# Performance work log

Measured on AMD Instinct MI355X. Metric: run time of the kernel, lower is better.

## Reference

```python
import jax, jax.numpy as jnp
import numpy as np

N_NODES = 100000


def _degrees(idx, n):
    d = jax.ops.segment_sum(jnp.ones(idx.shape[0], jnp.float32), idx, num_segments=n)
    return jnp.maximum(d, 1.0)  # DGL clamps zero degrees to 1


def graph_conv(src, dst, x, W, b, n):
    # DGL GraphConv with norm='both': out = D_in^{-1/2} A D_out^{-1/2} x W + b
    norm_src = _degrees(src, n) ** -0.5  # out-degree of source nodes
    norm_dst = _degrees(dst, n) ** -0.5  # in-degree of destination nodes
    xs = x * norm_src[:, None]
    msgs = xs[src]                                    # [E, d] gather
    agg = jax.ops.segment_sum(msgs, dst, num_segments=n)  # [N, d] scatter-add
    agg = agg * norm_dst[:, None]
    return agg @ W + b


def setup_inputs() -> dict:
    key = jax.random.key(0)
    k = jax.random.split(key, 7)
    E = 1600000
    in_f, h_f, out_f = 128, 128, 64
    return {
        "in_feat": jax.random.normal(k[0], (N_NODES, in_f), jnp.float32),
        "src": jax.random.randint(k[1], (E,), 0, N_NODES, jnp.int32),
        "dst": jax.random.randint(k[2], (E,), 0, N_NODES, jnp.int32),
        "W1": jax.random.normal(k[3], (in_f, h_f), jnp.float32) * (1.0 / np.sqrt(in_f)),
        "b1": jnp.zeros((h_f,), jnp.float32),
        "W2": jax.random.normal(k[4], (h_f, out_f), jnp.float32) * (1.0 / np.sqrt(h_f)),
        "b2": jnp.zeros((out_f,), jnp.float32),
    }


def reference(in_feat, src, dst, W1, b1, W2, b2):
    h = graph_conv(src, dst, in_feat, W1, b1, N_NODES)
    h = jax.nn.relu(h)
    h = graph_conv(src, dst, h, W2, b2, N_NODES)
    return h
```

## Files before the change

### kernel.cpp

```cpp
#include <hip/hip_runtime.h>

#define SLOT_CAP 64
#define NB_MAX 1024

__device__ __forceinline__ unsigned int bf16_rne(float f) {
    unsigned int u = __float_as_uint(f);
    return (u + 0x7FFFu + ((u >> 16) & 1u)) >> 16;
}
__device__ __forceinline__ unsigned int pack2(float a, float b) {
    return bf16_rne(a) | (bf16_rne(b) << 16);
}
__device__ __forceinline__ float bflo(unsigned int u) { return __uint_as_float(u << 16); }
__device__ __forceinline__ float bfhi(unsigned int u) { return __uint_as_float(u & 0xFFFF0000u); }

__global__ __launch_bounds__(256) void ka_kernel(
    const float* __restrict__ A, const float* __restrict__ W,
    unsigned short* __restrict__ C, int M,
    const int* __restrict__ src, const int* __restrict__ dst,
    int* __restrict__ bucket_cnt,
    int E, int GB, int NB)
{
    __shared__ __align__(16) int smem[32 * 68 + 32 * 128];
    const int tid = threadIdx.x;
    const int bid = blockIdx.x;

    if (bid >= GB) {
        const int eb = bid - GB;
        for (int b = tid; b < 2 * NB; b += 256) smem[b] = 0;
        __syncthreads();
        const int base = eb * 8192;
#pragma unroll
        for (int it = 0; it < 8; it++) {
            const int i4 = base + (it * 256 + tid) * 4;
            if (i4 + 3 < E) {
                int4 s = *(const int4*)(src + i4);
                int4 d = *(const int4*)(dst + i4);
                atomicAdd(&smem[d.x >> 7], 1); atomicAdd(&smem[d.y >> 7], 1);
                atomicAdd(&smem[d.z >> 7], 1); atomicAdd(&smem[d.w >> 7], 1);
                atomicAdd(&smem[NB + (s.x >> 7)], 1); atomicAdd(&smem[NB + (s.y >> 7)], 1);
                atomicAdd(&smem[NB + (s.z >> 7)], 1); atomicAdd(&smem[NB + (s.w >> 7)], 1);
            } else {
                for (int i = i4; i < E && i < i4 + 4; i++) {
                    atomicAdd(&smem[dst[i] >> 7], 1);
                    atomicAdd(&smem[NB + (src[i] >> 7)], 1);
                }
            }
        }
        __syncthreads();
        for (int b = tid; b < 2 * NB; b += 256) {
            int v = smem[b];
            if (v) atomicAdd(&bucket_cnt[b], v);
        }
        return;
    }

    float (*As2)[68] = (float(*)[68])smem;
    float* Ws = (float*)(smem + 32 * 68);
    const int row0 = bid * 64;
    if (row0 >= M) return;
    const int cx = tid & 31;
    const int ry = tid >> 5;
    const int kk = tid & 31;
    const int ri = tid >> 5;

    float acc[8][4];
#pragma unroll
    for (int r = 0; r < 8; r++)
#pragma unroll
        for (int c = 0; c < 4; c++) acc[r][c] = 0.0f;

    for (int k0 = 0; k0 < 128; k0 += 32) {
        __syncthreads();
#pragma unroll
        for (int jj = 0; jj < 8; jj++) {
            int r = ri + 8 * jj;
            int row = row0 + r;
            float v = 0.0f;
            if (row < M) v = A[(size_t)row * 128 + k0 + kk];
            As2[kk][r] = v;
        }
#pragma unroll
        for (int jj = 0; jj < 16; jj++) {
            int idx = tid + 256 * jj;
            Ws[idx] = W[k0 * 128 + idx];
        }
        __syncthreads();
#pragma unroll
        for (int k = 0; k < 32; k++) {
            float4 w = *(const float4*)&Ws[k * 128 + cx * 4];
            const float* ap = &As2[k][ry * 8];
            float4 a0 = *(const float4*)ap;
            float4 a1 = *(const float4*)(ap + 4);
            float a[8] = {a0.x, a0.y, a0.z, a0.w, a1.x, a1.y, a1.z, a1.w};
#pragma unroll
            for (int r = 0; r < 8; r++) {
                acc[r][0] = fmaf(a[r], w.x, acc[r][0]);
                acc[r][1] = fmaf(a[r], w.y, acc[r][1]);
                acc[r][2] = fmaf(a[r], w.z, acc[r][2]);
                acc[r][3] = fmaf(a[r], w.w, acc[r][3]);
            }
        }
    }
#pragma unroll
    for (int r = 0; r < 8; r++) {
        int row = row0 + ry * 8 + r;
        if (row < M) {
            uint2 p;
            p.x = pack2(acc[r][0], acc[r][1]);
            p.y = pack2(acc[r][2], acc[r][3]);
            *(uint2*)&C[(size_t)row * 128 + cx * 4] = p;
        }
    }
}

__global__ __launch_bounds__(256) void prefix_kernel(
    const int* __restrict__ bucket_cnt, int* __restrict__ bucket_base,
    int* __restrict__ bucket_cursor, int NB)
{
    __shared__ int tsum[256];
    const int off = blockIdx.x * NB;
    const int t = threadIdx.x;
    int v[4];
    int s = 0;
#pragma unroll
    for (int j = 0; j < 4; j++) {
        int b = t * 4 + j;
        v[j] = (b < NB) ? bucket_cnt[off + b] : 0;
        s += v[j];
    }
    tsum[t] = s;
    __syncthreads();
    for (int o = 1; o < 256; o <<= 1) {
        int x = (t >= o) ? tsum[t - o] : 0;
        __syncthreads();
        tsum[t] += x;
        __syncthreads();
    }
    int running = tsum[t] - s;
#pragma unroll
    for (int j = 0; j < 4; j++) {
        int b = t * 4 + j;
        if (b < NB) { bucket_base[off + b] = running; bucket_cursor[off + b] = running; }
        running += v[j];
    }
}

__global__ __launch_bounds__(256) void kb_kernel(
    const int* __restrict__ src, const int* __restrict__ dst,
    int* __restrict__ cursor,
    unsigned int* __restrict__ edge_shuf,
    unsigned char* __restrict__ src_shuf,
    int E, int NB)
{
    __shared__ int cntL[2 * NB_MAX];
    __shared__ int ofsL[2 * NB_MAX];
    const int tid = threadIdx.x;
    const int base = blockIdx.x * 8192;
    for (int b = tid; b < 2 * NB; b += 256) cntL[b] = 0;
    __syncthreads();
#pragma unroll
    for (int it = 0; it < 8; it++) {
        const int i4 = base + (it * 256 + tid) * 4;
        if (i4 + 3 < E) {
            int4 s = *(const int4*)(src + i4);
            int4 d = *(const int4*)(dst + i4);
            atomicAdd(&cntL[d.x >> 7], 1); atomicAdd(&cntL[d.y >> 7], 1);
            atomicAdd(&cntL[d.z >> 7], 1); atomicAdd(&cntL[d.w >> 7], 1);
            atomicAdd(&cntL[NB + (s.x >> 7)], 1); atomicAdd(&cntL[NB + (s.y >> 7)], 1);
            atomicAdd(&cntL[NB + (s.z >> 7)], 1); atomicAdd(&cntL[NB + (s.w >> 7)], 1);
        } else {
            for (int i = i4; i < E && i < i4 + 4; i++) {
                atomicAdd(&cntL[dst[i] >> 7], 1);
                atomicAdd(&cntL[NB + (src[i] >> 7)], 1);
            }
        }
    }
    __syncthreads();
    for (int b = tid; b < 2 * NB; b += 256) {
        int c = cntL[b];
        ofsL[b] = c ? atomicAdd(&cursor[b], c) : 0;
    }
    __syncthreads();
#pragma unroll
    for (int it = 0; it < 8; it++) {
        const int i4 = base + (it * 256 + tid) * 4;
        if (i4 + 3 < E) {
            int4 s = *(const int4*)(src + i4);
            int4 d = *(const int4*)(dst + i4);
            { int p = atomicAdd(&ofsL[d.x >> 7], 1); edge_shuf[p] = (unsigned)s.x | ((unsigned)(d.x & 127) << 17); }
            { int p = atomicAdd(&ofsL[d.y >> 7], 1); edge_shuf[p] = (unsigned)s.y | ((unsigned)(d.y & 127) << 17); }
            { int p = atomicAdd(&ofsL[d.z >> 7], 1); edge_shuf[p] = (unsigned)s.z | ((unsigned)(d.z & 127) << 17); }
            { int p = atomicAdd(&ofsL[d.w >> 7], 1); edge_shuf[p] = (unsigned)s.w | ((unsigned)(d.w & 127) << 17); }
            { int q = atomicAdd(&ofsL[NB + (s.x >> 7)], 1); src_shuf[q] = (unsigned char)(s.x & 127); }
            { int q = atomicAdd(&ofsL[NB + (s.y >> 7)], 1); src_shuf[q] = (unsigned char)(s.y & 127); }
            { int q = atomicAdd(&ofsL[NB + (s.z >> 7)], 1); src_shuf[q] = (unsigned char)(s.z & 127); }
            { int q = atomicAdd(&ofsL[NB + (s.w >> 7)], 1); src_shuf[q] = (unsigned char)(s.w & 127); }
        } else {
            for (int i = i4; i < E && i < i4 + 4; i++) {
                int sv = src[i], dv = dst[i];
                int p = atomicAdd(&ofsL[dv >> 7], 1);
                edge_shuf[p] = (unsigned)sv | ((unsigned)(dv & 127) << 17);
                int q = atomicAdd(&ofsL[NB + (sv >> 7)], 1);
                src_shuf[q] = (unsigned char)(sv & 127);
            }
        }
    }
}

__global__ __launch_bounds__(256) void kc_src_kernel(
    const unsigned char* __restrict__ src_shuf,
    const int* __restrict__ bucket_base, const int* __restrict__ bucket_cnt,
    int* __restrict__ cnt_src, int N)
{
    __shared__ int cntL[128];
    const int tid = threadIdx.x;
    const int b = blockIdx.x;
    if (tid < 128) cntL[tid] = 0;
    __syncthreads();
    const int start = bucket_base[b];
    const int len = bucket_cnt[b];
    for (int i = start + tid; i < start + len; i += 256)
        atomicAdd(&cntL[src_shuf[i]], 1);
    __syncthreads();
    if (tid < 128) {
        int node = b * 128 + tid;
        if (node < N) cnt_src[node] = cntL[tid];
    }
}

__global__ __launch_bounds__(256) void kc_dst_kernel(
    const unsigned int* __restrict__ edge_shuf,
    const int* __restrict__ bucket_base, const int* __restrict__ bucket_cnt,
    const int* __restrict__ cnt_src,
    int* __restrict__ cnt_dst, unsigned int* __restrict__ slots, int N)
{
    __shared__ int cntL[128];
    __shared__ unsigned int slotsL[128 * SLOT_CAP];
    const int tid = threadIdx.x;
    const int b = blockIdx.x;
    if (tid < 128) cntL[tid] = 0;
    __syncthreads();
    const int start = bucket_base[b];
    const int len = bucket_cnt[b];
    for (int i = start + tid; i < start + len; i += 256) {
        unsigned e = edge_shuf[i];
        int d = e >> 17;
        unsigned s = e & 0x1FFFFu;
        unsigned deg = (unsigned)min(cnt_src[s], 255);
        int r = atomicAdd(&cntL[d], 1);
        if (r < SLOT_CAP) slotsL[d * SLOT_CAP + r] = s | (deg << 17);
    }
    __syncthreads();
    if (tid < 128) {
        int node = b * 128 + tid;
        if (node < N) cnt_dst[node] = cntL[tid];
    }
    const int g = tid >> 4, lane = tid & 15;
    for (int nl = g; nl < 128; nl += 16) {
        int node = b * 128 + nl;
        if (node >= N) break;
        int len2 = min(cntL[nl], SLOT_CAP);
        for (int c = 0; c * 16 < len2; c++)
            slots[(size_t)node * SLOT_CAP + c * 16 + lane] = slotsL[nl * SLOT_CAP + c * 16 + lane];
    }
}

#define ACC8(V_, S_) \
    acc[0] = fmaf(bflo((V_).x), (S_), acc[0]); acc[1] = fmaf(bfhi((V_).x), (S_), acc[1]); \
    acc[2] = fmaf(bflo((V_).y), (S_), acc[2]); acc[3] = fmaf(bfhi((V_).y), (S_), acc[3]); \
    acc[4] = fmaf(bflo((V_).z), (S_), acc[4]); acc[5] = fmaf(bfhi((V_).z), (S_), acc[5]); \
    acc[6] = fmaf(bflo((V_).w), (S_), acc[6]); acc[7] = fmaf(bfhi((V_).w), (S_), acc[7]);

#define SUM8(V_) \
    acc[0] += bflo((V_).x); acc[1] += bfhi((V_).x); \
    acc[2] += bflo((V_).y); acc[3] += bfhi((V_).y); \
    acc[4] += bflo((V_).z); acc[5] += bfhi((V_).z); \
    acc[6] += bflo((V_).w); acc[7] += bfhi((V_).w);

__global__ __launch_bounds__(256) void pg2_kernel(
    const int* __restrict__ cnt_src, const int* __restrict__ cnt_dst,
    const unsigned int* __restrict__ slots, const unsigned int* __restrict__ msg,
    const float* __restrict__ W2, const float* __restrict__ b1,
    unsigned short* __restrict__ C, int N)
{
    __shared__ unsigned int Agp[64][66];
    __shared__ float Ws[32 * 64];
    const int tid = threadIdx.x;
    const int m0 = blockIdx.x * 64;
    const int lane = tid & 15;

#pragma unroll
    for (int p = 0; p < 4; p++) {
        const int nl = p * 16 + (tid >> 4);
        const int node = m0 + nl;
        float acc[8];
#pragma unroll
        for (int k = 0; k < 8; k++) acc[k] = 0.0f;
        if (node < N) {
            const unsigned int* sl = slots + (size_t)node * SLOT_CAP;
            const int cd = cnt_dst[node];
            const int len = min(cd, SLOT_CAP);
            int j = 0;
            for (; j + 7 < len; j += 8) {
                uint4 e0 = *(const uint4*)(sl + j);
                uint4 e1 = *(const uint4*)(sl + j + 4);
                uint4 a0 = *(const uint4*)(msg + (size_t)(e0.x & 0x1FFFFu) * 64 + lane * 4);
                uint4 a1 = *(const uint4*)(msg + (size_t)(e0.y & 0x1FFFFu) * 64 + lane * 4);
                uint4 a2 = *(const uint4*)(msg + (size_t)(e0.z & 0x1FFFFu) * 64 + lane * 4);
                uint4 a3 = *(const uint4*)(msg + (size_t)(e0.w & 0x1FFFFu) * 64 + lane * 4);
                uint4 a4 = *(const uint4*)(msg + (size_t)(e1.x & 0x1FFFFu) * 64 + lane * 4);
                uint4 a5 = *(const uint4*)(msg + (size_t)(e1.y & 0x1FFFFu) * 64 + lane * 4);
                uint4 a6 = *(const uint4*)(msg + (size_t)(e1.z & 0x1FFFFu) * 64 + lane * 4);
                uint4 a7 = *(const uint4*)(msg + (size_t)(e1.w & 0x1FFFFu) * 64 + lane * 4);
                float w0 = rsqrtf((float)(e0.x >> 17));
                float w1 = rsqrtf((float)(e0.y >> 17));
                float w2 = rsqrtf((float)(e0.z >> 17));
                float w3 = rsqrtf((float)(e0.w >> 17));
                float w4 = rsqrtf((float)(e1.x >> 17));
                float w5 = rsqrtf((float)(e1.y >> 17));
                float w6 = rsqrtf((float)(e1.z >> 17));
                float w7 = rsqrtf((float)(e1.w >> 17));
                ACC8(a0, w0) ACC8(a1, w1) ACC8(a2, w2) ACC8(a3, w3)
                ACC8(a4, w4) ACC8(a5, w5) ACC8(a6, w6) ACC8(a7, w7)
            }
            for (; j + 3 < len; j += 4) {
                uint4 e0 = *(const uint4*)(sl + j);
                uint4 a0 = *(const uint4*)(msg + (size_t)(e0.x & 0x1FFFFu) * 64 + lane * 4);
                uint4 a1 = *(const uint4*)(msg + (size_t)(e0.y & 0x1FFFFu) * 64 + lane * 4);
                uint4 a2 = *(const uint4*)(msg + (size_t)(e0.z & 0x1FFFFu) * 64 + lane * 4);
                uint4 a3 = *(const uint4*)(msg + (size_t)(e0.w & 0x1FFFFu) * 64 + lane * 4);
                float w0 = rsqrtf((float)(e0.x >> 17));
                float w1 = rsqrtf((float)(e0.y >> 17));
                float w2 = rsqrtf((float)(e0.z >> 17));
                float w3 = rsqrtf((float)(e0.w >> 17));
                ACC8(a0, w0) ACC8(a1, w1) ACC8(a2, w2) ACC8(a3, w3)
            }
            for (; j < len; j++) {
                unsigned e = sl[j];
                uint4 a0 = *(const uint4*)(msg + (size_t)(e & 0x1FFFFu) * 64 + lane * 4);
                float w0 = rsqrtf((float)(e >> 17));
                ACC8(a0, w0)
            }
            float nd = rsqrtf(fmaxf((float)cd, 1.0f));
            float ns = rsqrtf(fmaxf((float)cnt_src[node], 1.0f));
            float4 bA = *(const float4*)(b1 + lane * 8);
            float4 bB = *(const float4*)(b1 + lane * 8 + 4);
            acc[0] = fmaxf(fmaf(nd, acc[0], bA.x), 0.0f) * ns;
            acc[1] = fmaxf(fmaf(nd, acc[1], bA.y), 0.0f) * ns;
            acc[2] = fmaxf(fmaf(nd, acc[2], bA.z), 0.0f) * ns;
            acc[3] = fmaxf(fmaf(nd, acc[3], bA.w), 0.0f) * ns;
            acc[4] = fmaxf(fmaf(nd, acc[4], bB.x), 0.0f) * ns;
            acc[5] = fmaxf(fmaf(nd, acc[5], bB.y), 0.0f) * ns;
            acc[6] = fmaxf(fmaf(nd, acc[6], bB.z), 0.0f) * ns;
            acc[7] = fmaxf(fmaf(nd, acc[7], bB.w), 0.0f) * ns;
        }
        uint4 pk;
        pk.x = pack2(acc[0], acc[1]);
        pk.y = pack2(acc[2], acc[3]);
        pk.z = pack2(acc[4], acc[5]);
        pk.w = pack2(acc[6], acc[7]);
        *(uint4*)&Agp[nl][lane * 4] = pk;
    }
    __syncthreads();

    const int cx = tid & 15;
    const int rg = tid >> 4;
    float acc2[4][4];
#pragma unroll
    for (int r = 0; r < 4; r++)
#pragma unroll
        for (int c = 0; c < 4; c++) acc2[r][c] = 0.0f;

    for (int k0 = 0; k0 < 128; k0 += 32) {
#pragma unroll
        for (int jj = 0; jj < 8; jj++) {
            int idx = tid + 256 * jj;
            Ws[idx] = W2[k0 * 64 + idx];
        }
        __syncthreads();
#pragma unroll
        for (int kh = 0; kh < 16; kh++) {
            float4 wA = *(const float4*)&Ws[(2 * kh) * 64 + cx * 4];
            float4 wB = *(const float4*)&Ws[(2 * kh + 1) * 64 + cx * 4];
#pragma unroll
            for (int r = 0; r < 4; r++) {
                unsigned int u = Agp[rg * 4 + r][(k0 >> 1) + kh];
                float a0 = bflo(u), a1 = bfhi(u);
                acc2[r][0] = fmaf(a0, wA.x, acc2[r][0]);
                acc2[r][1] = fmaf(a0, wA.y, acc2[r][1]);
                acc2[r][2] = fmaf(a0, wA.z, acc2[r][2]);
                acc2[r][3] = fmaf(a0, wA.w, acc2[r][3]);
                acc2[r][0] = fmaf(a1, wB.x, acc2[r][0]);
                acc2[r][1] = fmaf(a1, wB.y, acc2[r][1]);
                acc2[r][2] = fmaf(a1, wB.z, acc2[r][2]);
                acc2[r][3] = fmaf(a1, wB.w, acc2[r][3]);
            }
        }
        __syncthreads();
    }
#pragma unroll
    for (int r = 0; r < 4; r++) {
        int row = m0 + rg * 4 + r;
        if (row < N) {
            uint2 p;
            p.x = pack2(acc2[r][0], acc2[r][1]);
            p.y = pack2(acc2[r][2], acc2[r][3]);
            *(uint2*)&C[(size_t)row * 64 + cx * 4] = p;
        }
    }
}

__global__ __launch_bounds__(256) void pull64_kernel(
    const int* __restrict__ cnt_dst, const unsigned int* __restrict__ slots,
    const unsigned int* __restrict__ msg,
    const float* __restrict__ b2, float* __restrict__ out, int N)
{
    const int t = blockIdx.x * 256 + threadIdx.x;
    const int node = t >> 3;
    const int lane = threadIdx.x & 7;
    if (node >= N) return;
    const unsigned int* sl = slots + (size_t)node * SLOT_CAP;
    const int cd = cnt_dst[node];
    const int len = min(cd, SLOT_CAP);
    float acc[8];
#pragma unroll
    for (int k = 0; k < 8; k++) acc[k] = 0.0f;
    int j = 0;
    for (; j + 7 < len; j += 8) {
        uint4 e0 = *(const uint4*)(sl + j);
        uint4 e1 = *(const uint4*)(sl + j + 4);
        uint4 a0 = *(const uint4*)(msg + (size_t)(e0.x & 0x1FFFFu) * 32 + lane * 4);
        uint4 a1 = *(const uint4*)(msg + (size_t)(e0.y & 0x1FFFFu) * 32 + lane * 4);
        uint4 a2 = *(const uint4*)(msg + (size_t)(e0.z & 0x1FFFFu) * 32 + lane * 4);
        uint4 a3 = *(const uint4*)(msg + (size_t)(e0.w & 0x1FFFFu) * 32 + lane * 4);
        uint4 a4 = *(const uint4*)(msg + (size_t)(e1.x & 0x1FFFFu) * 32 + lane * 4);
        uint4 a5 = *(const uint4*)(msg + (size_t)(e1.y & 0x1FFFFu) * 32 + lane * 4);
        uint4 a6 = *(const uint4*)(msg + (size_t)(e1.z & 0x1FFFFu) * 32 + lane * 4);
        uint4 a7 = *(const uint4*)(msg + (size_t)(e1.w & 0x1FFFFu) * 32 + lane * 4);
        SUM8(a0) SUM8(a1) SUM8(a2) SUM8(a3) SUM8(a4) SUM8(a5) SUM8(a6) SUM8(a7)
    }
    for (; j + 3 < len; j += 4) {
        uint4 e0 = *(const uint4*)(sl + j);
        uint4 a0 = *(const uint4*)(msg + (size_t)(e0.x & 0x1FFFFu) * 32 + lane * 4);
        uint4 a1 = *(const uint4*)(msg + (size_t)(e0.y & 0x1FFFFu) * 32 + lane * 4);
        uint4 a2 = *(const uint4*)(msg + (size_t)(e0.z & 0x1FFFFu) * 32 + lane * 4);
        uint4 a3 = *(const uint4*)(msg + (size_t)(e0.w & 0x1FFFFu) * 32 + lane * 4);
        SUM8(a0) SUM8(a1) SUM8(a2) SUM8(a3)
    }
    for (; j < len; j++) {
        unsigned e = sl[j];
        uint4 a0 = *(const uint4*)(msg + (size_t)(e & 0x1FFFFu) * 32 + lane * 4);
        SUM8(a0)
    }
    float nd = rsqrtf(fmaxf((float)cd, 1.0f));
    const float* bb = b2 + lane * 8;
    float4 bA = *(const float4*)(bb);
    float4 bB = *(const float4*)(bb + 4);
    float* o = out + (size_t)node * 64 + lane * 8;
    *(float4*)(o)     = make_float4(fmaf(acc[0], nd, bA.x), fmaf(acc[1], nd, bA.y),
                                    fmaf(acc[2], nd, bA.z), fmaf(acc[3], nd, bA.w));
    *(float4*)(o + 4) = make_float4(fmaf(acc[4], nd, bB.x), fmaf(acc[5], nd, bB.y),
                                    fmaf(acc[6], nd, bB.z), fmaf(acc[7], nd, bB.w));
}

extern "C" void kernel_launch(void* const* d_in, const int* in_sizes, int n_in,
                              void* d_out, int out_size, void* d_ws, size_t ws_size,
                              hipStream_t stream) {
    const float* x   = (const float*)d_in[0];
    const int*   src = (const int*)d_in[1];
    const int*   dst = (const int*)d_in[2];
    const float* W1  = (const float*)d_in[3];
    const float* b1  = (const float*)d_in[4];
    const float* W2  = (const float*)d_in[5];
    const float* b2  = (const float*)d_in[6];
    float* out = (float*)d_out;

    const int E = in_sizes[1];
    const int N = in_sizes[0] / 128;
    const int NB = (N + 127) >> 7;

    int* iws = (int*)d_ws;
    int* cnt_src     = iws;
    int* cnt_dst     = cnt_src + N;
    int* bucket_cnt  = cnt_dst + N;
    int* bucket_base = bucket_cnt + 2 * NB;
    int* bucket_cur  = bucket_base + 2 * NB;
    unsigned int* slots = (unsigned int*)(bucket_cur + 2 * NB);
    unsigned short* xw1 = (unsigned short*)(slots + (size_t)N * SLOT_CAP);
    unsigned short* hw2 = xw1 + (size_t)N * 128;
    unsigned int* edge_shuf = (unsigned int*)hw2;
    unsigned char* src_shuf = (unsigned char*)slots;

    hipMemsetAsync(bucket_cnt, 0, 2 * (size_t)NB * sizeof(int), stream);

    const int EB = (E + 8191) / 8192;
    const int GB = (N + 63) / 64;

    ka_kernel<<<GB + EB, 256, 0, stream>>>(
        x, W1, xw1, N, src, dst, bucket_cnt, E, GB, NB);

    prefix_kernel<<<2, 256, 0, stream>>>(bucket_cnt, bucket_base, bucket_cur, NB);

    kb_kernel<<<EB, 256, 0, stream>>>(src, dst, bucket_cur, edge_shuf, src_shuf, E, NB);

    kc_src_kernel<<<NB, 256, 0, stream>>>(src_shuf, bucket_base + NB, bucket_cnt + NB, cnt_src, N);

    kc_dst_kernel<<<NB, 256, 0, stream>>>(edge_shuf, bucket_base, bucket_cnt, cnt_src, cnt_dst, slots, N);

    pg2_kernel<<<(N + 63) / 64, 256, 0, stream>>>(
        cnt_src, cnt_dst, slots, (const unsigned int*)xw1, W2, b1, hw2, N);

    pull64_kernel<<<(N * 8 + 255) / 256, 256, 0, stream>>>(
        cnt_dst, slots, (const unsigned int*)hw2, b2, out, N);
}
```

Baseline: 370.2 us.

## Use split-bf16 MFMA for the first-layer X·W1 GEMM

Replaces the FP32 FMA register-tiled GEMM in ka_kernel with bf16 MFMA 16x16x32 instructions. A and W1 are each split into high and low bf16 parts, and three MFMAs per tile approximate FP32 accuracy. A small prep kernel transposes and splits W1 ahead of time. This moves the GEMM onto the matrix cores at the cost of an extra launch, more conversion ALU work, and scalar 16-bit output stores.

```diff
diff --git a/kernel.cpp b/kernel.cpp
--- a/kernel.cpp
+++ b/kernel.cpp
@@ -2,6 +2,9 @@
 
 #define SLOT_CAP 64
 #define NB_MAX 1024
+
+typedef __attribute__((ext_vector_type(8))) short bf16x8;
+typedef __attribute__((ext_vector_type(4))) float f32x4;
 
 __device__ __forceinline__ unsigned int bf16_rne(float f) {
     unsigned int u = __float_as_uint(f);
@@ -12,19 +15,34 @@
 }
 __device__ __forceinline__ float bflo(unsigned int u) { return __uint_as_float(u << 16); }
 __device__ __forceinline__ float bfhi(unsigned int u) { return __uint_as_float(u & 0xFFFF0000u); }
+__device__ __forceinline__ float bf16val(unsigned int h) { return __uint_as_float(h << 16); }
+
+__global__ __launch_bounds__(256) void prep_w_kernel(
+    const float* __restrict__ W1, unsigned short* __restrict__ wt_hi,
+    unsigned short* __restrict__ wt_lo)
+{
+    const int idx = blockIdx.x * 256 + threadIdx.x;
+    const int c = idx >> 7, k = idx & 127;
+    float v = W1[k * 128 + c];
+    unsigned int h = bf16_rne(v);
+    wt_hi[idx] = (unsigned short)h;
+    wt_lo[idx] = (unsigned short)bf16_rne(v - bf16val(h));
+}
 
 __global__ __launch_bounds__(256) void ka_kernel(
-    const float* __restrict__ A, const float* __restrict__ W,
+    const float* __restrict__ A,
+    const unsigned short* __restrict__ wt_hi_g, const unsigned short* __restrict__ wt_lo_g,
     unsigned short* __restrict__ C, int M,
     const int* __restrict__ src, const int* __restrict__ dst,
     int* __restrict__ bucket_cnt,
     int E, int GB, int NB)
 {
-    __shared__ __align__(16) int smem[32 * 68 + 32 * 128];
+    __shared__ __align__(16) unsigned short smem_us[2 * 64 * 40 + 2 * 128 * 40];
     const int tid = threadIdx.x;
     const int bid = blockIdx.x;
 
     if (bid >= GB) {
+        int* smem = (int*)smem_us;
         const int eb = bid - GB;
         for (int b = tid; b < 2 * NB; b += 256) smem[b] = 0;
         __syncthreads();
@@ -54,61 +72,74 @@
         return;
     }
 
-    float (*As2)[68] = (float(*)[68])smem;
-    float* Ws = (float*)(smem + 32 * 68);
+    unsigned short* As_hi = smem_us;
+    unsigned short* As_lo = As_hi + 64 * 40;
+    unsigned short* Ws_hi = As_lo + 64 * 40;
+    unsigned short* Ws_lo = Ws_hi + 128 * 40;
+
     const int row0 = bid * 64;
     if (row0 >= M) return;
-    const int cx = tid & 31;
-    const int ry = tid >> 5;
-    const int kk = tid & 31;
-    const int ri = tid >> 5;
-
-    float acc[8][4];
-#pragma unroll
-    for (int r = 0; r < 8; r++)
-#pragma unroll
-        for (int c = 0; c < 4; c++) acc[r][c] = 0.0f;
+    const int wv = tid >> 6;
+    const int ln = tid & 63;
+    const int fr = ln & 15;
+    const int fk = ln >> 4;
+
+    f32x4 acc[8];
+#pragma unroll
+    for (int t = 0; t < 8; t++) acc[t] = (f32x4){0.0f, 0.0f, 0.0f, 0.0f};
+
+    const int sr = tid >> 2;
+    const int sq = (tid & 3) * 8;
 
     for (int k0 = 0; k0 < 128; k0 += 32) {
         __syncthreads();
-#pragma unroll
-        for (int jj = 0; jj < 8; jj++) {
-            int r = ri + 8 * jj;
-            int row = row0 + r;
-            float v = 0.0f;
-            if (row < M) v = A[(size_t)row * 128 + k0 + kk];
-            As2[kk][r] = v;
-        }
-#pragma unroll
-        for (int jj = 0; jj < 16; jj++) {
-            int idx = tid + 256 * jj;
-            Ws[idx] = W[k0 * 128 + idx];
-        }
-        __syncthreads();
-#pragma unroll
-        for (int k = 0; k < 32; k++) {
-            float4 w = *(const float4*)&Ws[k * 128 + cx * 4];
-            const float* ap = &As2[k][ry * 8];
-            float4 a0 = *(const float4*)ap;
-            float4 a1 = *(const float4*)(ap + 4);
-            float a[8] = {a0.x, a0.y, a0.z, a0.w, a1.x, a1.y, a1.z, a1.w};
-#pragma unroll
-            for (int r = 0; r < 8; r++) {
-                acc[r][0] = fmaf(a[r], w.x, acc[r][0]);
-                acc[r][1] = fmaf(a[r], w.y, acc[r][1]);
-                acc[r][2] = fmaf(a[r], w.z, acc[r][2]);
-                acc[r][3] = fmaf(a[r], w.w, acc[r][3]);
-            }
-        }
-    }
-#pragma unroll
-    for (int r = 0; r < 8; r++) {
-        int row = row0 + ry * 8 + r;
-        if (row < M) {
-            uint2 p;
-            p.x = pack2(acc[r][0], acc[r][1]);
-            p.y = pack2(acc[r][2], acc[r][3]);
-            *(uint2*)&C[(size_t)row * 128 + cx * 4] = p;
+        {
+            const int row = row0 + sr;
+            float v0 = 0, v1 = 0, v2 = 0, v3 = 0, v4 = 0, v5 = 0, v6 = 0, v7 = 0;
+            if (row < M) {
+                const float4 p0 = *(const float4*)&A[(size_t)row * 128 + k0 + sq];
+                const float4 p1 = *(const float4*)&A[(size_t)row * 128 + k0 + sq + 4];
+                v0 = p0.x; v1 = p0.y; v2 = p0.z; v3 = p0.w;
+                v4 = p1.x; v5 = p1.y; v6 = p1.z; v7 = p1.w;
+            }
+            unsigned int h0 = bf16_rne(v0), h1 = bf16_rne(v1), h2 = bf16_rne(v2), h3 = bf16_rne(v3);
+            unsigned int h4 = bf16_rne(v4), h5 = bf16_rne(v5), h6 = bf16_rne(v6), h7 = bf16_rne(v7);
+            uint4 hi, lo;
+            hi.x = h0 | (h1 << 16); hi.y = h2 | (h3 << 16);
+            hi.z = h4 | (h5 << 16); hi.w = h6 | (h7 << 16);
+            lo.x = bf16_rne(v0 - bf16val(h0)) | (bf16_rne(v1 - bf16val(h1)) << 16);
+            lo.y = bf16_rne(v2 - bf16val(h2)) | (bf16_rne(v3 - bf16val(h3)) << 16);
+            lo.z = bf16_rne(v4 - bf16val(h4)) | (bf16_rne(v5 - bf16val(h5)) << 16);
+            lo.w = bf16_rne(v6 - bf16val(h6)) | (bf16_rne(v7 - bf16val(h7)) << 16);
+            *(uint4*)&As_hi[sr * 40 + sq] = hi;
+            *(uint4*)&As_lo[sr * 40 + sq] = lo;
+        }
+#pragma unroll
+        for (int j = 0; j < 8; j++) {
+            int idx = tid + 256 * j;
+            int c = idx >> 4, k2 = (idx & 15) * 2;
+            *(unsigned int*)&Ws_hi[c * 40 + k2] = *(const unsigned int*)&wt_hi_g[c * 128 + k0 + k2];
+            *(unsigned int*)&Ws_lo[c * 40 + k2] = *(const unsigned int*)&wt_lo_g[c * 128 + k0 + k2];
+        }
+        __syncthreads();
+
+        bf16x8 ah = *(const bf16x8*)&As_hi[(16 * wv + fr) * 40 + fk * 8];
+        bf16x8 al = *(const bf16x8*)&As_lo[(16 * wv + fr) * 40 + fk * 8];
+#pragma unroll
+        for (int t = 0; t < 8; t++) {
+            bf16x8 bh = *(const bf16x8*)&Ws_hi[(16 * t + fr) * 40 + fk * 8];
+            bf16x8 bl = *(const bf16x8*)&Ws_lo[(16 * t + fr) * 40 + fk * 8];
+            acc[t] = __builtin_amdgcn_mfma_f32_16x16x32_bf16(ah, bh, acc[t], 0, 0, 0);
+            acc[t] = __builtin_amdgcn_mfma_f32_16x16x32_bf16(al, bh, acc[t], 0, 0, 0);
+            acc[t] = __builtin_amdgcn_mfma_f32_16x16x32_bf16(ah, bl, acc[t], 0, 0, 0);
+        }
+    }
+#pragma unroll
+    for (int t = 0; t < 8; t++) {
+#pragma unroll
+        for (int rg = 0; rg < 4; rg++) {
+            int row = row0 + 16 * wv + fk * 4 + rg;
+            if (row < M) C[(size_t)row * 128 + 16 * t + fr] = (unsigned short)bf16_rne(acc[t][rg]);
         }
     }
 }
@@ -488,6 +519,8 @@
     unsigned int* slots = (unsigned int*)(bucket_cur + 2 * NB);
     unsigned short* xw1 = (unsigned short*)(slots + (size_t)N * SLOT_CAP);
     unsigned short* hw2 = xw1 + (size_t)N * 128;
+    unsigned short* wt_hi = hw2 + (size_t)N * 64;
+    unsigned short* wt_lo = wt_hi + 128 * 128;
     unsigned int* edge_shuf = (unsigned int*)hw2;
     unsigned char* src_shuf = (unsigned char*)slots;
 
@@ -496,8 +529,10 @@
     const int EB = (E + 8191) / 8192;
     const int GB = (N + 63) / 64;
 
+    prep_w_kernel<<<64, 256, 0, stream>>>(W1, wt_hi, wt_lo);
+
     ka_kernel<<<GB + EB, 256, 0, stream>>>(
-        x, W1, xw1, N, src, dst, bucket_cnt, E, GB, NB);
+        x, wt_hi, wt_lo, xw1, N, src, dst, bucket_cnt, E, GB, NB);
 
     prefix_kernel<<<2, 256, 0, stream>>>(bucket_cnt, bucket_base, bucket_cur, NB);
 
```

Measured after the change: 344.4 us. -7.0%, faster.
